# Performance work log

Measured on AMD Instinct MI355X. Metric: run time of the kernel, lower is better.

The kernel has to match this reference:

```python
import jax, jax.numpy as jnp
import numpy as np

LEAK = 0.9  # leaky-integrator rate of the ESN cell


def setup_inputs() -> dict:
    key = jax.random.key(0)
    ks = jax.random.split(key, 7)
    S, B, I, R = 512, 64, 256, 2048
    sc_in0 = 1.0 / np.sqrt(I)
    sc_h = 0.9 / np.sqrt(R)  # ~spectral-radius style scaling
    sc_in1 = 1.0 / np.sqrt(R)
    return {
        "x": jax.random.normal(ks[0], (S, B, I), jnp.float32),
        "W_in0": jax.random.normal(ks[1], (R, I), jnp.float32) * sc_in0,
        "W_hh0": jax.random.normal(ks[2], (R, R), jnp.float32) * sc_h,
        "b0": jax.random.normal(ks[3], (R,), jnp.float32) * 0.1,
        "W_in1": jax.random.normal(ks[4], (R, R), jnp.float32) * sc_in1,
        "W_hh1": jax.random.normal(ks[5], (R, R), jnp.float32) * sc_h,
        "b1": jax.random.normal(ks[6], (R,), jnp.float32) * 0.1,
    }


def _esn_layer(x_seq, W_in, W_hh, b):
    # x_seq: (S, B, D_in); returns (S, B, R), (B, R)
    B = x_seq.shape[1]
    R = W_hh.shape[0]
    h0 = jnp.zeros((B, R), x_seq.dtype)
    # Precompute input projection for all timesteps in one big GEMM.
    xin = jnp.einsum('sbd,rd->sbr', x_seq, W_in) + b

    def step(h, xin_t):
        h_new = (1.0 - LEAK) * h + LEAK * jnp.tanh(xin_t + h @ W_hh.T)
        return h_new, h_new

    h_n, ys = jax.lax.scan(step, h0, xin)
    return ys, h_n


def reference(x, W_in0, W_hh0, b0, W_in1, W_hh1, b1):
    y0, h0n = _esn_layer(x, W_in0, W_hh0, b0)
    y1, h1n = _esn_layer(y0, W_in1, W_hh1, b1)
    h_n = jnp.stack([h0n, h1n])  # (num_layers, B, R)
    return y1, h_n
```

## Files before the change

### kernel.cpp

```cpp
#include <hip/hip_runtime.h>

typedef _Float16 half8 __attribute__((ext_vector_type(8)));
typedef float floatx4 __attribute__((ext_vector_type(4)));

#define S_LEN 512
#define NB 64
#define NI 256
#define NR 2048
#define LEAK 0.9f

#define NBLK 128
#define TPB 512
#define LBLK 64
#define NBNR ((size_t)NB * NR)

#define CHT0 72
#define CHT1 128

#define OFF_BAR ((size_t)0)
#define OFF_H0  ((size_t)4096)
#define OFF_H1  (OFF_H0 + 2 * NBNR * 2)
#define OFF_XE  (OFF_H1 + 2 * NBNR * 2)
#define SZ_XE   ((size_t)S_LEN * NB * NI * 2)
#define OFF_W0  (OFF_XE + SZ_XE)
#define SZ_W0   ((size_t)128 * CHT0 * 1024)
#define OFF_W1  (OFF_W0 + SZ_W0)
#define SZ_W1   ((size_t)128 * CHT1 * 1024)
#define WS_NEED (OFF_W1 + SZ_W1)

__device__ __forceinline__ half8 cvt8(const float* s) {
    float4 p = *(const float4*)s, q = *(const float4*)(s + 4);
    half8 v;
    v[0] = (_Float16)p.x; v[1] = (_Float16)p.y; v[2] = (_Float16)p.z; v[3] = (_Float16)p.w;
    v[4] = (_Float16)q.x; v[5] = (_Float16)q.y; v[6] = (_Float16)q.z; v[7] = (_Float16)q.w;
    return v;
}

__global__ void xprep_kernel(const float* __restrict__ x, _Float16* __restrict__ xe) {
    const int t = blockIdx.x;
    #pragma unroll
    for (int it = 0; it < 4; ++it) {
        const int u = it * 8 + (threadIdx.x >> 6);
        const int l = threadIdx.x & 63;
        const int b = (u >> 3) * 16 + (l & 15);
        const int i0 = (u & 7) * 32 + (l >> 4) * 8;
        half8 v = cvt8(x + ((size_t)t * NB + b) * NI + i0);
        *(half8*)(xe + (size_t)t * NB * NI + (size_t)u * 512 + (size_t)l * 8) = v;
    }
}

__global__ void wprep_kernel(const float* __restrict__ Whh0, const float* __restrict__ Win0,
                             const float* __restrict__ Whh1, const float* __restrict__ Win1,
                             _Float16* __restrict__ w0f, _Float16* __restrict__ w1f) {
    int unit = blockIdx.x * 4 + (threadIdx.x >> 6);
    const int l = threadIdx.x & 63;
    const float* Whh; const float* Win; _Float16* dst; int CHT, KU;
    if (unit < 128 * CHT0) { Whh = Whh0; Win = Win0; dst = w0f; CHT = CHT0; KU = NI; }
    else { unit -= 128 * CHT0; Whh = Whh1; Win = Win1; dst = w1f; CHT = CHT1; KU = NR; }
    const int fg = unit / CHT, ch = unit - fg * CHT;
    const int feat = fg * 16 + (l & 15);
    const int k = ch * 32 + (l >> 4) * 8;
    const float* src = (k < NR) ? Whh + (size_t)feat * NR + k
                                : Win + (size_t)feat * KU + (k - NR);
    *(half8*)(dst + ((size_t)unit << 9) + (size_t)l * 8) = cvt8(src);
}

__device__ __forceinline__ void gbar(unsigned* bar) {
    __syncthreads();
    if (threadIdx.x == 0) {
        __threadfence();
        unsigned* cnt  = bar + (blockIdx.x & 7) * 32;
        unsigned* root = bar + 256;
        unsigned* gen  = bar + 272;
        unsigned g = __hip_atomic_load(gen, __ATOMIC_RELAXED, __HIP_MEMORY_SCOPE_AGENT);
        bool last = false;
        if (__hip_atomic_fetch_add(cnt, 1u, __ATOMIC_ACQ_REL, __HIP_MEMORY_SCOPE_AGENT) == (NBLK / 8 - 1)) {
            __hip_atomic_store(cnt, 0u, __ATOMIC_RELAXED, __HIP_MEMORY_SCOPE_AGENT);
            if (__hip_atomic_fetch_add(root, 1u, __ATOMIC_ACQ_REL, __HIP_MEMORY_SCOPE_AGENT) == 7u) {
                __hip_atomic_store(root, 0u, __ATOMIC_RELAXED, __HIP_MEMORY_SCOPE_AGENT);
                __hip_atomic_store(gen, g + 1u, __ATOMIC_RELEASE, __HIP_MEMORY_SCOPE_AGENT);
                last = true;
            }
        }
        if (!last)
            while (__hip_atomic_load(gen, __ATOMIC_RELAXED, __HIP_MEMORY_SCOPE_AGENT) == g)
                __builtin_amdgcn_s_sleep(1);
        __threadfence();
    }
    __syncthreads();
}

__device__ __forceinline__ void stage8(half8* d, const char* src, int unitbase, int l) {
    #pragma unroll
    for (int jj = 0; jj < 8; ++jj)
        d[jj] = *(const half8*)(src + ((size_t)(unitbase + jj) << 10) + (size_t)l * 16);
}

template <int ROLE, bool WF16>
__device__ __forceinline__ void esn_layer_run(
    const float* __restrict__ bias_v,
    const float* Whh, const float* Win,
    const _Float16* __restrict__ wf,
    const char* __restrict__ xe,
    char* hp, const char* h0p,
    float* __restrict__ out,
    unsigned* __restrict__ bar,
    float* __restrict__ rsc, int r0)
{
    const int tid = threadIdx.x;
    const int l = tid & 63, w = tid >> 6, l15 = l & 15, g = l >> 4;
    constexpr int CHT = ROLE ? CHT1 : CHT0;
    const int fg0 = r0 >> 4;

    const int fg_o = w & 1, bt_o = w >> 1;
    const int ncol = r0 + fg_o * 16 + l15;
    const int bj0 = bt_o * 16 + g * 4;
    const float bias = bias_v[ncol];
    const int cu = ncol >> 5, gg = (ncol >> 3) & 3, ee = ncol & 7;
    float hs[4] = {0.f, 0.f, 0.f, 0.f};
    float* hn_base = out + (size_t)S_LEN * NBNR + (size_t)ROLE * NBNR;

    for (int s = 0; s < S_LEN + 1; ++s) {
        const int t = (ROLE == 0) ? s : s - 1;
        const bool active = (ROLE == 0) ? (s < S_LEN) : (s >= 1);
        if (active) {
            const char* hu = hp + (size_t)(t & 1) * (NBNR * 2);
            const char* uu = (ROLE == 0) ? xe + (size_t)t * NB * NI * 2
                                         : h0p + (size_t)((t + 1) & 1) * (NBNR * 2);

            floatx4 acc[2][4];
            #pragma unroll
            for (int fg = 0; fg < 2; ++fg)
                #pragma unroll
                for (int bt = 0; bt < 4; ++bt)
                    acc[fg][bt] = (floatx4){0.f, 0.f, 0.f, 0.f};

            half8 wA[8], wB[8], ab[2][8];

            if (WF16) {
                const _Float16* p0 = wf + (((size_t)fg0 * CHT + w * 8) << 9) + (size_t)l * 8;
                const _Float16* p1 = wf + (((size_t)(fg0 + 1) * CHT + w * 8) << 9) + (size_t)l * 8;
                #pragma unroll
                for (int jj = 0; jj < 8; ++jj) {
                    wA[jj] = *(const half8*)(p0 + ((size_t)jj << 9));
                    wB[jj] = *(const half8*)(p1 + ((size_t)jj << 9));
                }
            } else {
                #pragma unroll
                for (int jj = 0; jj < 8; ++jj) {
                    wA[jj] = cvt8(Whh + (size_t)(r0 + l15) * NR + (w * 8 + jj) * 32 + g * 8);
                    wB[jj] = cvt8(Whh + (size_t)(r0 + 16 + l15) * NR + (w * 8 + jj) * 32 + g * 8);
                }
            }
            stage8(ab[0], hu, w * 8, l);
            #pragma unroll
            for (int bt = 0; bt < 4; ++bt) {
                if (bt < 3) stage8(ab[(bt + 1) & 1], hu, (bt + 1) * 64 + w * 8, l);
                #pragma unroll
                for (int jj = 0; jj < 8; ++jj) {
                    acc[0][bt] = __builtin_amdgcn_mfma_f32_16x16x32_f16(ab[bt & 1][jj], wA[jj], acc[0][bt], 0, 0, 0);
                    acc[1][bt] = __builtin_amdgcn_mfma_f32_16x16x32_f16(ab[bt & 1][jj], wB[jj], acc[1][bt], 0, 0, 0);
                }
            }

            if (ROLE == 1) {
                if (WF16) {
                    const _Float16* p0 = wf + (((size_t)fg0 * CHT + 64 + w * 8) << 9) + (size_t)l * 8;
                    const _Float16* p1 = wf + (((size_t)(fg0 + 1) * CHT + 64 + w * 8) << 9) + (size_t)l * 8;
                    #pragma unroll
                    for (int jj = 0; jj < 8; ++jj) {
                        wA[jj] = *(const half8*)(p0 + ((size_t)jj << 9));
                        wB[jj] = *(const half8*)(p1 + ((size_t)jj << 9));
                    }
                } else {
                    #pragma unroll
                    for (int jj = 0; jj < 8; ++jj) {
                        wA[jj] = cvt8(Win + (size_t)(r0 + l15) * NR + (w * 8 + jj) * 32 + g * 8);
                        wB[jj] = cvt8(Win + (size_t)(r0 + 16 + l15) * NR + (w * 8 + jj) * 32 + g * 8);
                    }
                }
                stage8(ab[0], uu, w * 8, l);
                #pragma unroll
                for (int bt = 0; bt < 4; ++bt) {
                    if (bt < 3) stage8(ab[(bt + 1) & 1], uu, (bt + 1) * 64 + w * 8, l);
                    #pragma unroll
                    for (int jj = 0; jj < 8; ++jj) {
                        acc[0][bt] = __builtin_amdgcn_mfma_f32_16x16x32_f16(ab[bt & 1][jj], wA[jj], acc[0][bt], 0, 0, 0);
                        acc[1][bt] = __builtin_amdgcn_mfma_f32_16x16x32_f16(ab[bt & 1][jj], wB[jj], acc[1][bt], 0, 0, 0);
                    }
                }
            } else {
                half8 wiA, wiB, ai[4];
                if (WF16) {
                    wiA = *(const half8*)(wf + (((size_t)fg0 * CHT + 64 + w) << 9) + (size_t)l * 8);
                    wiB = *(const half8*)(wf + (((size_t)(fg0 + 1) * CHT + 64 + w) << 9) + (size_t)l * 8);
                } else {
                    wiA = cvt8(Win + (size_t)(r0 + l15) * NI + w * 32 + g * 8);
                    wiB = cvt8(Win + (size_t)(r0 + 16 + l15) * NI + w * 32 + g * 8);
                }
                #pragma unroll
                for (int bt = 0; bt < 4; ++bt)
                    ai[bt] = *(const half8*)(uu + ((size_t)(bt * 8 + w) << 10) + (size_t)l * 16);
                #pragma unroll
                for (int bt = 0; bt < 4; ++bt) {
                    acc[0][bt] = __builtin_amdgcn_mfma_f32_16x16x32_f16(ai[bt], wiA, acc[0][bt], 0, 0, 0);
                    acc[1][bt] = __builtin_amdgcn_mfma_f32_16x16x32_f16(ai[bt], wiB, acc[1][bt], 0, 0, 0);
                }
            }

            #pragma unroll
            for (int fg = 0; fg < 2; ++fg)
                #pragma unroll
                for (int bt = 0; bt < 4; ++bt)
                    *(floatx4*)(rsc + (size_t)((w * 8 + fg * 4 + bt) * 64 + l) * 4) = acc[fg][bt];
            __syncthreads();

            floatx4 r = {0.f, 0.f, 0.f, 0.f};
            #pragma unroll
            for (int v = 0; v < 8; ++v)
                r += *(const floatx4*)(rsc + (size_t)((v * 8 + fg_o * 4 + bt_o) * 64 + l) * 4);

            char* hw = hp + (size_t)((t + 1) & 1) * (NBNR * 2);
            #pragma unroll
            for (int j = 0; j < 4; ++j) {
                float hn = (1.0f - LEAK) * hs[j] + LEAK * tanhf(r[j] + bias);
                hs[j] = hn;
                const int bj = bj0 + j;
                size_t byte = (size_t)((bj >> 4) * 64 + cu) * 1024
                            + (size_t)((gg * 16 + (bj & 15)) * 8 + ee) * 2;
                *(_Float16*)(hw + byte) = (_Float16)hn;
                if (ROLE == 1)
                    __builtin_nontemporal_store(hn, out + (size_t)t * NBNR + (size_t)bj * NR + ncol);
                if (t == S_LEN - 1)
                    __builtin_nontemporal_store(hn, hn_base + (size_t)bj * NR + ncol);
            }
        }
        if (s < S_LEN) gbar(bar);
    }
}

template <bool WF16>
__global__ void __launch_bounds__(TPB, 1) esn_kernel(
    const float* __restrict__ b0v, const float* __restrict__ b1v,
    const float* Whh0, const float* Win0,
    const float* Whh1, const float* Win1,
    const _Float16* __restrict__ w0f, const _Float16* __restrict__ w1f,
    const char* __restrict__ xe,
    char* h0p, char* h1p,
    unsigned* __restrict__ bar, float* __restrict__ out)
{
    __shared__ __align__(16) float rsc[64 * 64 * 4];
    const int bid = blockIdx.x;
    if (bid < LBLK)
        esn_layer_run<0, WF16>(b0v, Whh0, Win0, w0f, xe, h0p, nullptr,
                               out, bar, rsc, bid * 32);
    else
        esn_layer_run<1, WF16>(b1v, Whh1, Win1, w1f, nullptr, h1p, h0p,
                               out, bar, rsc, (bid - LBLK) * 32);
}

extern "C" void kernel_launch(void* const* d_in, const int* in_sizes, int n_in,
                              void* d_out, int out_size, void* d_ws, size_t ws_size,
                              hipStream_t stream) {
    const float* x    = (const float*)d_in[0];
    const float* Win0 = (const float*)d_in[1];
    const float* Whh0 = (const float*)d_in[2];
    const float* b0   = (const float*)d_in[3];
    const float* Win1 = (const float*)d_in[4];
    const float* Whh1 = (const float*)d_in[5];
    const float* b1   = (const float*)d_in[6];

    char* ws = (char*)d_ws;
    char* xe  = ws + OFF_XE;
    char* h0p = ws + OFF_H0;
    char* h1p = ws + OFF_H1;
    unsigned* bar = (unsigned*)(ws + OFF_BAR);
    _Float16* w0f = (_Float16*)(ws + OFF_W0);
    _Float16* w1f = (_Float16*)(ws + OFF_W1);
    float* out = (float*)d_out;

    const bool wf16 = (ws_size >= WS_NEED);

    (void)hipMemsetAsync(ws, 0, OFF_XE, stream);
    xprep_kernel<<<dim3(S_LEN), dim3(512), 0, stream>>>(x, (_Float16*)xe);
    if (wf16)
        wprep_kernel<<<dim3((128 * (CHT0 + CHT1)) / 4), dim3(256), 0, stream>>>(
            Whh0, Win0, Whh1, Win1, w0f, w1f);

    void* args[] = { (void*)&b0, (void*)&b1, (void*)&Whh0, (void*)&Win0,
                     (void*)&Whh1, (void*)&Win1, (void*)&w0f, (void*)&w1f,
                     (void*)&xe, (void*)&h0p, (void*)&h1p, (void*)&bar, (void*)&out };
    void* fn = wf16 ? (void*)esn_kernel<true> : (void*)esn_kernel<false>;
    hipError_t e = hipLaunchCooperativeKernel(fn, dim3(NBLK), dim3(TPB),
                                              args, 0, stream);
    if (e != hipSuccess) {
        if (wf16)
            esn_kernel<true><<<dim3(NBLK), dim3(TPB), 0, stream>>>(
                b0, b1, Whh0, Win0, Whh1, Win1, w0f, w1f, xe, h0p, h1p, bar, out);
        else
            esn_kernel<false><<<dim3(NBLK), dim3(TPB), 0, stream>>>(
                b0, b1, Whh0, Win0, Whh1, Win1, w0f, w1f, xe, h0p, h1p, bar, out);
    }
}
```

Baseline: 9.593 ms.

## Relax grid barrier fences and prefetch recurrent weights before barrier

```diff
diff --git a/kernel.cpp b/kernel.cpp
--- a/kernel.cpp
+++ b/kernel.cpp
@@ -65,16 +65,21 @@
     *(half8*)(dst + ((size_t)unit << 9) + (size_t)l * 8) = cvt8(src);
 }
 
+__device__ __forceinline__ void stH(_Float16* p, _Float16 v) {
+    unsigned short b;
+    __builtin_memcpy(&b, &v, 2);
+    __hip_atomic_store((unsigned short*)p, b, __ATOMIC_RELAXED, __HIP_MEMORY_SCOPE_AGENT);
+}
+
 __device__ __forceinline__ void gbar(unsigned* bar) {
     __syncthreads();
     if (threadIdx.x == 0) {
-        __threadfence();
         unsigned* cnt  = bar + (blockIdx.x & 7) * 32;
         unsigned* root = bar + 256;
         unsigned* gen  = bar + 272;
         unsigned g = __hip_atomic_load(gen, __ATOMIC_RELAXED, __HIP_MEMORY_SCOPE_AGENT);
         bool last = false;
-        if (__hip_atomic_fetch_add(cnt, 1u, __ATOMIC_ACQ_REL, __HIP_MEMORY_SCOPE_AGENT) == (NBLK / 8 - 1)) {
+        if (__hip_atomic_fetch_add(cnt, 1u, __ATOMIC_RELAXED, __HIP_MEMORY_SCOPE_AGENT) == (NBLK / 8 - 1)) {
             __hip_atomic_store(cnt, 0u, __ATOMIC_RELAXED, __HIP_MEMORY_SCOPE_AGENT);
             if (__hip_atomic_fetch_add(root, 1u, __ATOMIC_ACQ_REL, __HIP_MEMORY_SCOPE_AGENT) == 7u) {
                 __hip_atomic_store(root, 0u, __ATOMIC_RELAXED, __HIP_MEMORY_SCOPE_AGENT);
@@ -85,9 +90,9 @@
         if (!last)
             while (__hip_atomic_load(gen, __ATOMIC_RELAXED, __HIP_MEMORY_SCOPE_AGENT) == g)
                 __builtin_amdgcn_s_sleep(1);
-        __threadfence();
     }
     __syncthreads();
+    __builtin_amdgcn_fence(__ATOMIC_ACQUIRE, "agent");
 }
 
 __device__ __forceinline__ void stage8(half8* d, const char* src, int unitbase, int l) {
@@ -120,77 +125,68 @@
     float hs[4] = {0.f, 0.f, 0.f, 0.f};
     float* hn_base = out + (size_t)S_LEN * NBNR + (size_t)ROLE * NBNR;
 
+    half8 wA0[8], wB0[8];
+    half8 ai[4];
+
+    auto loadW0 = [&]() {
+        if (WF16) {
+            const _Float16* p0 = wf + (((size_t)fg0 * CHT + w * 8) << 9) + (size_t)l * 8;
+            const _Float16* p1 = wf + (((size_t)(fg0 + 1) * CHT + w * 8) << 9) + (size_t)l * 8;
+            #pragma unroll
+            for (int jj = 0; jj < 8; ++jj) {
+                wA0[jj] = *(const half8*)(p0 + ((size_t)jj << 9));
+                wB0[jj] = *(const half8*)(p1 + ((size_t)jj << 9));
+            }
+        } else {
+            #pragma unroll
+            for (int jj = 0; jj < 8; ++jj) {
+                wA0[jj] = cvt8(Whh + (size_t)(r0 + l15) * NR + (w * 8 + jj) * 32 + g * 8);
+                wB0[jj] = cvt8(Whh + (size_t)(r0 + 16 + l15) * NR + (w * 8 + jj) * 32 + g * 8);
+            }
+        }
+        #pragma unroll
+        for (int jj = 0; jj < 8; ++jj)
+            asm volatile("" : "+v"(wA0[jj]), "+v"(wB0[jj]));
+    };
+    auto loadU0 = [&](int t) {
+        const char* uu = xe + (size_t)t * NB * NI * 2;
+        #pragma unroll
+        for (int bt = 0; bt < 4; ++bt)
+            ai[bt] = *(const half8*)(uu + ((size_t)(bt * 8 + w) << 10) + (size_t)l * 16);
+        #pragma unroll
+        for (int bt = 0; bt < 4; ++bt)
+            asm volatile("" : "+v"(ai[bt]));
+    };
+
+    loadW0();
+    if (ROLE == 0) loadU0(0);
+
     for (int s = 0; s < S_LEN + 1; ++s) {
         const int t = (ROLE == 0) ? s : s - 1;
         const bool active = (ROLE == 0) ? (s < S_LEN) : (s >= 1);
         if (active) {
             const char* hu = hp + (size_t)(t & 1) * (NBNR * 2);
-            const char* uu = (ROLE == 0) ? xe + (size_t)t * NB * NI * 2
+            const char* uu = (ROLE == 0) ? nullptr
                                          : h0p + (size_t)((t + 1) & 1) * (NBNR * 2);
 
-            floatx4 acc[2][4];
-            #pragma unroll
-            for (int fg = 0; fg < 2; ++fg)
-                #pragma unroll
-                for (int bt = 0; bt < 4; ++bt)
-                    acc[fg][bt] = (floatx4){0.f, 0.f, 0.f, 0.f};
-
-            half8 wA[8], wB[8], ab[2][8];
-
-            if (WF16) {
-                const _Float16* p0 = wf + (((size_t)fg0 * CHT + w * 8) << 9) + (size_t)l * 8;
-                const _Float16* p1 = wf + (((size_t)(fg0 + 1) * CHT + w * 8) << 9) + (size_t)l * 8;
-                #pragma unroll
-                for (int jj = 0; jj < 8; ++jj) {
-                    wA[jj] = *(const half8*)(p0 + ((size_t)jj << 9));
-                    wB[jj] = *(const half8*)(p1 + ((size_t)jj << 9));
-                }
-            } else {
-                #pragma unroll
-                for (int jj = 0; jj < 8; ++jj) {
-                    wA[jj] = cvt8(Whh + (size_t)(r0 + l15) * NR + (w * 8 + jj) * 32 + g * 8);
-                    wB[jj] = cvt8(Whh + (size_t)(r0 + 16 + l15) * NR + (w * 8 + jj) * 32 + g * 8);
-                }
-            }
-            stage8(ab[0], hu, w * 8, l);
-            #pragma unroll
-            for (int bt = 0; bt < 4; ++bt) {
-                if (bt < 3) stage8(ab[(bt + 1) & 1], hu, (bt + 1) * 64 + w * 8, l);
-                #pragma unroll
-                for (int jj = 0; jj < 8; ++jj) {
-                    acc[0][bt] = __builtin_amdgcn_mfma_f32_16x16x32_f16(ab[bt & 1][jj], wA[jj], acc[0][bt], 0, 0, 0);
-                    acc[1][bt] = __builtin_amdgcn_mfma_f32_16x16x32_f16(ab[bt & 1][jj], wB[jj], acc[1][bt], 0, 0, 0);
-                }
-            }
-
+            half8 wA1[8], wB1[8], wiA, wiB;
             if (ROLE == 1) {
                 if (WF16) {
                     const _Float16* p0 = wf + (((size_t)fg0 * CHT + 64 + w * 8) << 9) + (size_t)l * 8;
                     const _Float16* p1 = wf + (((size_t)(fg0 + 1) * CHT + 64 + w * 8) << 9) + (size_t)l * 8;
                     #pragma unroll
                     for (int jj = 0; jj < 8; ++jj) {
-                        wA[jj] = *(const half8*)(p0 + ((size_t)jj << 9));
-                        wB[jj] = *(const half8*)(p1 + ((size_t)jj << 9));
+                        wA1[jj] = *(const half8*)(p0 + ((size_t)jj << 9));
+                        wB1[jj] = *(const half8*)(p1 + ((size_t)jj << 9));
                     }
                 } else {
                     #pragma unroll
                     for (int jj = 0; jj < 8; ++jj) {
-                        wA[jj] = cvt8(Win + (size_t)(r0 + l15) * NR + (w * 8 + jj) * 32 + g * 8);
-                        wB[jj] = cvt8(Win + (size_t)(r0 + 16 + l15) * NR + (w * 8 + jj) * 32 + g * 8);
+                        wA1[jj] = cvt8(Win + (size_t)(r0 + l15) * NR + (w * 8 + jj) * 32 + g * 8);
+                        wB1[jj] = cvt8(Win + (size_t)(r0 + 16 + l15) * NR + (w * 8 + jj) * 32 + g * 8);
                     }
                 }
-                stage8(ab[0], uu, w * 8, l);
-                #pragma unroll
-                for (int bt = 0; bt < 4; ++bt) {
-                    if (bt < 3) stage8(ab[(bt + 1) & 1], uu, (bt + 1) * 64 + w * 8, l);
-                    #pragma unroll
-                    for (int jj = 0; jj < 8; ++jj) {
-                        acc[0][bt] = __builtin_amdgcn_mfma_f32_16x16x32_f16(ab[bt & 1][jj], wA[jj], acc[0][bt], 0, 0, 0);
-                        acc[1][bt] = __builtin_amdgcn_mfma_f32_16x16x32_f16(ab[bt & 1][jj], wB[jj], acc[1][bt], 0, 0, 0);
-                    }
-                }
             } else {
-                half8 wiA, wiB, ai[4];
                 if (WF16) {
                     wiA = *(const half8*)(wf + (((size_t)fg0 * CHT + 64 + w) << 9) + (size_t)l * 8);
                     wiB = *(const half8*)(wf + (((size_t)(fg0 + 1) * CHT + 64 + w) << 9) + (size_t)l * 8);
@@ -198,15 +194,49 @@
                     wiA = cvt8(Win + (size_t)(r0 + l15) * NI + w * 32 + g * 8);
                     wiB = cvt8(Win + (size_t)(r0 + 16 + l15) * NI + w * 32 + g * 8);
                 }
+            }
+
+            floatx4 acc[2][4];
+            #pragma unroll
+            for (int fg = 0; fg < 2; ++fg)
                 #pragma unroll
                 for (int bt = 0; bt < 4; ++bt)
-                    ai[bt] = *(const half8*)(uu + ((size_t)(bt * 8 + w) << 10) + (size_t)l * 16);
+                    acc[fg][bt] = (floatx4){0.f, 0.f, 0.f, 0.f};
+
+            half8 ab[2][8];
+
+            stage8(ab[0], hu, w * 8, l);
+            #pragma unroll
+            for (int bt = 0; bt < 4; ++bt) {
+                if (bt < 3) stage8(ab[(bt + 1) & 1], hu, (bt + 1) * 64 + w * 8, l);
+                #pragma unroll
+                for (int jj = 0; jj < 8; ++jj) {
+                    acc[0][bt] = __builtin_amdgcn_mfma_f32_16x16x32_f16(ab[bt & 1][jj], wA0[jj], acc[0][bt], 0, 0, 0);
+                    acc[1][bt] = __builtin_amdgcn_mfma_f32_16x16x32_f16(ab[bt & 1][jj], wB0[jj], acc[1][bt], 0, 0, 0);
+                }
+            }
+
+            if (ROLE == 1) {
+                stage8(ab[0], uu, w * 8, l);
+                #pragma unroll
+                for (int bt = 0; bt < 4; ++bt) {
+                    if (bt < 3) stage8(ab[(bt + 1) & 1], uu, (bt + 1) * 64 + w * 8, l);
+                    #pragma unroll
+                    for (int jj = 0; jj < 8; ++jj) {
+                        acc[0][bt] = __builtin_amdgcn_mfma_f32_16x16x32_f16(ab[bt & 1][jj], wA1[jj], acc[0][bt], 0, 0, 0);
+                        acc[1][bt] = __builtin_amdgcn_mfma_f32_16x16x32_f16(ab[bt & 1][jj], wB1[jj], acc[1][bt], 0, 0, 0);
+                    }
+                }
+            } else {
                 #pragma unroll
                 for (int bt = 0; bt < 4; ++bt) {
                     acc[0][bt] = __builtin_amdgcn_mfma_f32_16x16x32_f16(ai[bt], wiA, acc[0][bt], 0, 0, 0);
                     acc[1][bt] = __builtin_amdgcn_mfma_f32_16x16x32_f16(ai[bt], wiB, acc[1][bt], 0, 0, 0);
                 }
             }
+
+            loadW0();
+            if (ROLE == 0) loadU0((t + 1 < S_LEN) ? t + 1 : t);
 
             #pragma unroll
             for (int fg = 0; fg < 2; ++fg)
@@ -228,7 +258,7 @@
                 const int bj = bj0 + j;
                 size_t byte = (size_t)((bj >> 4) * 64 + cu) * 1024
                             + (size_t)((gg * 16 + (bj & 15)) * 8 + ee) * 2;
-                *(_Float16*)(hw + byte) = (_Float16)hn;
+                stH((_Float16*)(hw + byte), (_Float16)hn);
                 if (ROLE == 1)
                     __builtin_nontemporal_store(hn, out + (size_t)t * NBNR + (size_t)bj * NR + ncol);
                 if (t == S_LEN - 1)
```

Result: slower. 9.847 ms (+2.7%).
